# Performance work log

Hardware: AMD Instinct MI355X
Metric: run time of the kernel (lower is better)

## Reference

```python
import jax, jax.numpy as jnp
import numpy as np

D = 256    # lstm_encoder_size
B = 1024   # batch (number of agents/trajectories)
T = 512    # prediction horizon (recurrence steps)
EPS = 1e-5


def setup_inputs() -> dict:
    key = jax.random.key(0)
    k = jax.random.split(key, 10)
    s = 1.0 / np.sqrt(D)
    return {
        "KS_ALL": jax.random.normal(k[0], (1, B, D), jnp.float32),
        "next_vf": jax.random.normal(k[1], (B, T), jnp.float32),
        # Koopman operators (torch Linear stores [out, in]; no bias)
        "A_w": jax.random.normal(k[2], (D, D), jnp.float32) * (0.4 * s),  # contractive
        "B_w": jax.random.normal(k[3], (D, 1), jnp.float32) * s,
        # decoder params (liner_dec=False)
        "W0": jax.random.normal(k[4], (2 * D, D), jnp.float32) * s,
        "b0": jnp.zeros((2 * D,), jnp.float32),
        "W1": jax.random.normal(k[5], (D, 2 * D), jnp.float32) / np.sqrt(2.0 * D),
        "b1": jnp.zeros((D,), jnp.float32),
        "ln_g": jnp.ones((D,), jnp.float32),
        "ln_b": jnp.zeros((D,), jnp.float32),
        "W2": jax.random.normal(k[6], (D, D), jnp.float32) * s,
        "b2": jnp.zeros((D,), jnp.float32),
        "W3": jax.random.normal(k[7], (3, D), jnp.float32) * s,
        "b3": jnp.zeros((3,), jnp.float32),
    }


def _layer_norm(x, g, b):
    mu = jnp.mean(x, axis=-1, keepdims=True)
    var = jnp.var(x, axis=-1, keepdims=True)
    return (x - mu) * jax.lax.rsqrt(var + EPS) * g + b


def reference(KS_ALL, next_vf, A_w, B_w, W0, b0, W1, b1, ln_g, ln_b, W2, b2, W3, b3):
    # train_flag=True -> use only the first time slice of KS_ALL
    ks0 = KS_ALL[0]                 # [B, D]
    u = next_vf.T                   # [T, B] time-major, matches permute(1,0,2)
    b_vec = B_w[:, 0]               # [D]  (Linear(1, D) on scalar input)

    def step(ks, u_t):
        ks_new = ks @ A_w.T + u_t[:, None] * b_vec[None, :]  # [B, D]
        return ks_new, ks_new

    _, ks_seq = jax.lax.scan(step, ks0, u)                   # [T, B, D]
    KS_pre = jnp.concatenate([ks0[None], ks_seq], axis=0)    # [T+1, B, D]

    # nonlinear decoder (eval mode: dropout is identity; use_elu=True)
    s1 = jnp.tanh(KS_pre @ W0.T + b0)          # [T+1, B, 2D]
    s2 = jnp.tanh(s1 @ W1.T + b1)              # [T+1, B, D]
    s2 = _layer_norm(KS_pre + s2, ln_g, ln_b)  # AddAndNorm
    s3 = jax.nn.elu(s2 @ W2.T + b2)
    OS = s3 @ W3.T + b3                        # [T+1, B, 3]
    return KS_pre, OS
```

## Files before the change

### kernel.cpp

```cpp
#include <hip/hip_runtime.h>

typedef unsigned short u16;
typedef __attribute__((ext_vector_type(8))) short bf16x8;
typedef __attribute__((ext_vector_type(4))) short bf16x4;
typedef __attribute__((ext_vector_type(4))) float f32x4;

#define MFMA16(a, b, c) __builtin_amdgcn_mfma_f32_16x16x32_bf16((a), (b), (c), 0, 0, 0)

#define OFF_UPAD 0
#define OFF_KS0  589824
#define OFF_W0   851968
#define OFF_W1   983040
#define OFF_W2   1114112
#define OFF_CRT  1179648
#define OFF_P    1196032
#define OS_OFF   134479872

__device__ __forceinline__ u16 f2bf(float f) {
  union { float f; unsigned int i; } v; v.f = f;
  return (u16)((v.i + 0x7fffu + ((v.i >> 16) & 1u)) >> 16);
}
__device__ __forceinline__ float bf2f(u16 u) {
  union { unsigned int i; float f; } v; v.i = ((unsigned int)u) << 16;
  return v.f;
}
__device__ __forceinline__ float fast_tanh(float x) {
  float e = __expf(2.0f * x);
  return 1.0f - __fdividef(2.0f, e + 1.0f);
}

__global__ void k_prep(const float* __restrict__ KS_ALL, const float* __restrict__ next_vf,
                       const float* __restrict__ A_w, const float* __restrict__ W0,
                       const float* __restrict__ W1, const float* __restrict__ W2,
                       u16* __restrict__ ws) {
  int idx = blockIdx.x * 256 + threadIdx.x;
  if (idx < 589824) {
    int r = idx / 576, c = idx % 576;
    ws[OFF_UPAD + idx] = (c < 64) ? (u16)0 : f2bf(next_vf[r * 512 + c - 64]);
    return;
  }
  idx -= 589824;
  if (idx < 262144) { ws[OFF_KS0 + idx] = f2bf(KS_ALL[idx]); return; }
  idx -= 262144;
  if (idx < 131072) { ws[OFF_W0 + idx] = f2bf(W0[idx]); return; }
  idx -= 131072;
  if (idx < 131072) { ws[OFF_W1 + idx] = f2bf(W1[idx]); return; }
  idx -= 131072;
  if (idx < 65536)  { ws[OFF_W2 + idx] = f2bf(W2[idx]); return; }
  idx -= 65536;
  if (idx < 65536) {
    int r = idx >> 8, c = idx & 255;
    ws[OFF_P + idx] = (r == c) ? (u16)0x3F80 : (u16)0;
    ws[OFF_P + 65536 + idx] = f2bf(A_w[idx]);
  }
}

__global__ __launch_bounds__(512) void k_pow(u16* __restrict__ ws, int s) {
  const u16* P = ws + OFF_P;
  int j = blockIdx.y + 1;
  int mh = blockIdx.x;
  int lane = threadIdx.x & 63, w = threadIdx.x >> 6;
  int wm = w >> 2, wn = w & 3;
  int lg = lane >> 4, ll = lane & 15;
  const u16* Am = P + s * 65536;
  const u16* Bm = P + j * 65536;
  f32x4 acc[4][4];
  f32x4 z = {0.f, 0.f, 0.f, 0.f};
#pragma unroll
  for (int mi = 0; mi < 4; ++mi)
#pragma unroll
    for (int ni = 0; ni < 4; ++ni) acc[mi][ni] = z;
#pragma unroll
  for (int ks = 0; ks < 8; ++ks) {
    bf16x8 a[4], b[4];
    int kk = ks * 32 + lg * 8;
#pragma unroll
    for (int mi = 0; mi < 4; ++mi) {
      int row = mh * 128 + wm * 64 + mi * 16 + ll;
      a[mi] = *(const bf16x8*)(Am + row * 256 + kk);
    }
#pragma unroll
    for (int ni = 0; ni < 4; ++ni) {
      int col = wn * 64 + ni * 16 + ll;
#pragma unroll
      for (int e = 0; e < 8; ++e) b[ni][e] = (short)Bm[(kk + e) * 256 + col];
    }
#pragma unroll
    for (int mi = 0; mi < 4; ++mi)
#pragma unroll
      for (int ni = 0; ni < 4; ++ni) acc[mi][ni] = MFMA16(a[mi], b[ni], acc[mi][ni]);
  }
  u16* Pd = ws + OFF_P + (s + j) * 65536;
#pragma unroll
  for (int mi = 0; mi < 4; ++mi)
#pragma unroll
    for (int ni = 0; ni < 4; ++ni)
#pragma unroll
      for (int r = 0; r < 4; ++r) {
        int row = mh * 128 + wm * 64 + mi * 16 + lg * 4 + r;
        int col = wn * 64 + ni * 16 + ll;
        Pd[row * 256 + col] = f2bf(acc[mi][ni][r]);
      }
}

__global__ void k_crevt(const float* __restrict__ B_w, u16* __restrict__ ws) {
  int s = blockIdx.x;
  int n = threadIdx.x;
  const u16* Pr = ws + OFF_P + (63 - s) * 65536 + n * 256;
  float acc = 0.f;
  for (int k = 0; k < 256; ++k) acc += bf2f(Pr[k]) * B_w[k];
  ws[OFF_CRT + n * 64 + s] = f2bf(acc);
}

__global__ __launch_bounds__(512) void k_fused(
    const u16* __restrict__ ws,
    const float* __restrict__ b0, const float* __restrict__ b1,
    const float* __restrict__ lng, const float* __restrict__ lnb,
    const float* __restrict__ b2, const float* __restrict__ W3,
    const float* __restrict__ b3, float* __restrict__ out) {
  __shared__ __align__(16) u16 Xb[16896];
  __shared__ __align__(16) unsigned char Hraw[33792];
  __shared__ float par[2308];
  u16* Hb = (u16*)Hraw;
  float* Hf = (float*)Hraw;

  float* pb0 = par;
  float* pb1 = par + 512;
  float* pg  = par + 768;
  float* pbt = par + 1024;
  float* pb2 = par + 1280;
  float* pW3 = par + 1536;
  float* pb3 = par + 2304;

  const int t  = blockIdx.y;
  const int R0 = blockIdx.x * 64;
  const int tid = threadIdx.x;
  const int lane = tid & 63, w = tid >> 6;
  const int lg = lane >> 4, ll = lane & 15;

  pb0[tid] = b0[tid];
  if (tid < 256) { pb1[tid] = b1[tid]; pg[tid] = lng[tid]; pbt[tid] = lnb[tid]; pb2[tid] = b2[tid]; }
  if (tid < 512) pW3[tid] = W3[tid];
  if (tid < 256) pW3[512 + tid] = W3[512 + tid];
  if (tid < 4) pb3[tid] = (tid < 3) ? b3[tid] : 0.f;

  f32x4 z = {0.f, 0.f, 0.f, 0.f};

  f32x4 acc[4][2];
#pragma unroll
  for (int mi = 0; mi < 4; ++mi)
#pragma unroll
    for (int ni = 0; ni < 2; ++ni) acc[mi][ni] = z;
  {
    const u16* CrevT = ws + OFF_CRT;
#pragma unroll
    for (int ksu = 0; ksu < 2; ++ksu) {
      bf16x8 au[4];
#pragma unroll
      for (int mi = 0; mi < 4; ++mi) {
        const u16* up = ws + OFF_UPAD + (R0 + mi * 16 + ll) * 576 + t + ksu * 32 + lg * 8;
#pragma unroll
        for (int e = 0; e < 8; ++e) au[mi][e] = (short)up[e];
      }
#pragma unroll
      for (int ni = 0; ni < 2; ++ni) {
        int n = w * 32 + ni * 16 + ll;
        bf16x8 bfr = *(const bf16x8*)(CrevT + n * 64 + ksu * 32 + lg * 8);
#pragma unroll
        for (int mi = 0; mi < 4; ++mi) acc[mi][ni] = MFMA16(au[mi], bfr, acc[mi][ni]);
      }
    }
    if (t < 64) {
      const u16* Pt = ws + OFF_P + t * 65536;
      const u16* ks0b = ws + OFF_KS0;
#pragma unroll
      for (int ks = 0; ks < 8; ++ks) {
        bf16x8 a[4], b[2];
#pragma unroll
        for (int mi = 0; mi < 4; ++mi)
          a[mi] = *(const bf16x8*)(ks0b + (R0 + mi * 16 + ll) * 256 + ks * 32 + lg * 8);
#pragma unroll
        for (int ni = 0; ni < 2; ++ni)
          b[ni] = *(const bf16x8*)(Pt + (w * 32 + ni * 16 + ll) * 256 + ks * 32 + lg * 8);
#pragma unroll
        for (int mi = 0; mi < 4; ++mi)
#pragma unroll
          for (int ni = 0; ni < 2; ++ni) acc[mi][ni] = MFMA16(a[mi], b[ni], acc[mi][ni]);
      }
    }
  }

#pragma unroll 1
  for (int p = 0; p < 2; ++p) {
#pragma unroll
    for (int mi2 = 0; mi2 < 2; ++mi2) {
      int mi = p * 2 + mi2;
#pragma unroll
      for (int ni = 0; ni < 2; ++ni)
#pragma unroll
        for (int r = 0; r < 4; ++r)
          Hf[(mi2 * 16 + lg * 4 + r) * 260 + w * 32 + ni * 16 + ll] = acc[mi][ni][r];
    }
    __syncthreads();
    float* ob = out + (size_t)t * 262144 + (size_t)(R0 + p * 32) * 256;
#pragma unroll
    for (int it = 0; it < 4; ++it) {
      int idx = it * 512 + tid;
      int row = idx >> 6, c4 = idx & 63;
      f32x4 v = *(const f32x4*)(Hf + row * 260 + c4 * 4);
      *(f32x4*)(ob + row * 256 + c4 * 4) = v;
      int rl = p * 32 + row;
      bf16x4 h;
#pragma unroll
      for (int e = 0; e < 4; ++e) h[e] = (short)f2bf(v[e]);
      int byt = (((rl << 9) + ((c4 >> 1) << 4)) ^ ((rl & 7) << 4)) + ((c4 & 1) << 3);
      *(bf16x4*)(Xb + (byt >> 1)) = h;
    }
    __syncthreads();
  }

  const u16* W0b = ws + OFF_W0;
  const u16* W1b = ws + OFF_W1;
  f32x4 accL2[4][2];
#pragma unroll
  for (int mi = 0; mi < 4; ++mi)
#pragma unroll
    for (int ni = 0; ni < 2; ++ni) accL2[mi][ni] = z;

  const int colL1 = w * 16 + ll;
#pragma unroll 1
  for (int q = 0; q < 4; ++q) {
    f32x4 accQ[4];
#pragma unroll
    for (int mi = 0; mi < 4; ++mi) accQ[mi] = z;
#pragma unroll
    for (int ks = 0; ks < 8; ++ks) {
      bf16x8 b = *(const bf16x8*)(W0b + (q * 128 + colL1) * 256 + ks * 32 + lg * 8);
#pragma unroll
      for (int mi = 0; mi < 4; ++mi) {
        int rl = mi * 16 + ll;
        int byt = ((rl << 9) + ks * 64 + (lg << 4)) ^ ((rl & 7) << 4);
        bf16x8 a = *(const bf16x8*)(Xb + (byt >> 1));
        accQ[mi] = MFMA16(a, b, accQ[mi]);
      }
    }
#pragma unroll
    for (int mi = 0; mi < 4; ++mi)
#pragma unroll
      for (int r = 0; r < 4; ++r) {
        int rl2 = mi * 16 + lg * 4 + r;
        float v = fast_tanh(accQ[mi][r] + pb0[q * 128 + colL1]);
        int byt = ((rl2 << 8) + (colL1 << 1)) ^ ((rl2 & 7) << 4);
        Hb[byt >> 1] = f2bf(v);
      }
    __syncthreads();
#pragma unroll
    for (int ks2 = 0; ks2 < 4; ++ks2) {
      bf16x8 bf0 = *(const bf16x8*)(W1b + (w * 32 + ll) * 512 + q * 128 + ks2 * 32 + lg * 8);
      bf16x8 bf1 = *(const bf16x8*)(W1b + (w * 32 + 16 + ll) * 512 + q * 128 + ks2 * 32 + lg * 8);
#pragma unroll
      for (int mi = 0; mi < 4; ++mi) {
        int rl = mi * 16 + ll;
        int byt = ((rl << 8) + ks2 * 64 + (lg << 4)) ^ ((rl & 7) << 4);
        bf16x8 a = *(const bf16x8*)(Hb + (byt >> 1));
        accL2[mi][0] = MFMA16(a, bf0, accL2[mi][0]);
        accL2[mi][1] = MFMA16(a, bf1, accL2[mi][1]);
      }
    }
    __syncthreads();
  }

#pragma unroll
  for (int mi = 0; mi < 4; ++mi)
#pragma unroll
    for (int ni = 0; ni < 2; ++ni)
#pragma unroll
      for (int r = 0; r < 4; ++r) {
        int rl = mi * 16 + lg * 4 + r;
        int col = w * 32 + ni * 16 + ll;
        float v = fast_tanh(accL2[mi][ni][r] + pb1[col]);
        int bx = ((rl << 9) + (col << 1)) ^ ((rl & 7) << 4);
        v += bf2f(Xb[bx >> 1]);
        Hb[rl * 264 + col] = f2bf(v);
      }
  __syncthreads();

  {
    int row = tid >> 3, jq = tid & 7;
    u16* hr = Hb + row * 264 + jq * 32;
    bf16x8 chv[4];
#pragma unroll
    for (int q = 0; q < 4; ++q) chv[q] = *(const bf16x8*)(hr + q * 8);
    float s = 0.f, ss = 0.f;
#pragma unroll
    for (int q = 0; q < 4; ++q)
#pragma unroll
      for (int e = 0; e < 8; ++e) { float v = bf2f((u16)chv[q][e]); s += v; ss += v * v; }
    s += __shfl_xor(s, 1);  s += __shfl_xor(s, 2);  s += __shfl_xor(s, 4);
    ss += __shfl_xor(ss, 1); ss += __shfl_xor(ss, 2); ss += __shfl_xor(ss, 4);
    float mu = s * 0.00390625f;
    float var = ss * 0.00390625f - mu * mu;
    float rstd = rsqrtf(var + 1e-5f);
#pragma unroll
    for (int q = 0; q < 4; ++q) {
      bf16x8 o;
#pragma unroll
      for (int e = 0; e < 8; ++e) {
        int col = jq * 32 + q * 8 + e;
        float v = (bf2f((u16)chv[q][e]) - mu) * rstd * pg[col] + pbt[col];
        o[e] = (short)f2bf(v);
      }
      *(bf16x8*)(hr + q * 8) = o;
    }
  }
  __syncthreads();

  {
    const u16* W2b = ws + OFF_W2;
    f32x4 a3[4][2];
#pragma unroll
    for (int mi = 0; mi < 4; ++mi)
#pragma unroll
      for (int ni = 0; ni < 2; ++ni) a3[mi][ni] = z;
#pragma unroll
    for (int ks = 0; ks < 8; ++ks) {
      bf16x8 bf0 = *(const bf16x8*)(W2b + (w * 32 + ll) * 256 + ks * 32 + lg * 8);
      bf16x8 bf1 = *(const bf16x8*)(W2b + (w * 32 + 16 + ll) * 256 + ks * 32 + lg * 8);
#pragma unroll
      for (int mi = 0; mi < 4; ++mi) {
        int rl = mi * 16 + ll;
        bf16x8 a = *(const bf16x8*)(Hb + rl * 264 + ks * 32 + lg * 8);
        a3[mi][0] = MFMA16(a, bf0, a3[mi][0]);
        a3[mi][1] = MFMA16(a, bf1, a3[mi][1]);
      }
    }
#pragma unroll
    for (int mi = 0; mi < 4; ++mi)
#pragma unroll
      for (int ni = 0; ni < 2; ++ni)
#pragma unroll
        for (int r = 0; r < 4; ++r) {
          int rl = mi * 16 + lg * 4 + r;
          int col = w * 32 + ni * 16 + ll;
          float v = a3[mi][ni][r] + pb2[col];
          v = v > 0.f ? v : (__expf(v) - 1.f);
          Xb[rl * 264 + col] = f2bf(v);
        }
  }
  __syncthreads();

  {
    int row = tid >> 3, jq = tid & 7;
    const u16* xr = Xb + row * 264 + jq * 32;
    float d0 = 0.f, d1 = 0.f, d2 = 0.f;
#pragma unroll
    for (int q = 0; q < 4; ++q) {
      bf16x8 c = *(const bf16x8*)(xr + q * 8);
#pragma unroll
      for (int e = 0; e < 8; ++e) {
        float v = bf2f((u16)c[e]);
        int col = jq * 32 + q * 8 + e;
        d0 += v * pW3[col]; d1 += v * pW3[256 + col]; d2 += v * pW3[512 + col];
      }
    }
    d0 += __shfl_xor(d0, 1); d0 += __shfl_xor(d0, 2); d0 += __shfl_xor(d0, 4);
    d1 += __shfl_xor(d1, 1); d1 += __shfl_xor(d1, 2); d1 += __shfl_xor(d1, 4);
    d2 += __shfl_xor(d2, 1); d2 += __shfl_xor(d2, 2); d2 += __shfl_xor(d2, 4);
    if (jq == 0) {
      int grow = R0 + row;
      int ob = OS_OFF + t * 3072 + grow * 3;
      out[ob]     = d0 + pb3[0];
      out[ob + 1] = d1 + pb3[1];
      out[ob + 2] = d2 + pb3[2];
    }
  }
}

extern "C" void kernel_launch(void* const* d_in, const int* in_sizes, int n_in,
                              void* d_out, int out_size, void* d_ws, size_t ws_size,
                              hipStream_t stream) {
  const float* KS_ALL  = (const float*)d_in[0];
  const float* next_vf = (const float*)d_in[1];
  const float* A_w     = (const float*)d_in[2];
  const float* B_w     = (const float*)d_in[3];
  const float* W0      = (const float*)d_in[4];
  const float* b0      = (const float*)d_in[5];
  const float* W1      = (const float*)d_in[6];
  const float* b1      = (const float*)d_in[7];
  const float* lng     = (const float*)d_in[8];
  const float* lnb     = (const float*)d_in[9];
  const float* W2      = (const float*)d_in[10];
  const float* b2      = (const float*)d_in[11];
  const float* W3      = (const float*)d_in[12];
  const float* b3      = (const float*)d_in[13];
  u16* ws = (u16*)d_ws;
  float* out = (float*)d_out;

  k_prep<<<4864, 256, 0, stream>>>(KS_ALL, next_vf, A_w, W0, W1, W2, ws);
  for (int s = 1; s <= 32; s <<= 1)
    k_pow<<<dim3(2, s), 512, 0, stream>>>(ws, s);
  k_crevt<<<64, 256, 0, stream>>>(B_w, ws);
  k_fused<<<dim3(16, 513), 512, 0, stream>>>(ws, b0, b1, lng, lnb, b2, W3, b3, out);
}
```

Measured before the change: 1.604 ms.

## Split fused decoder kernel into KS, layer1, layer2, layer3 kernels over time chunks

Replaces the single fused kernel with a KS-sequence kernel and three per-layer decoder kernels, run over four time chunks. Intermediates (tanh layer-1 output, layer-normed activations) are staged in bf16 workspace buffers. The aim is lower register and LDS pressure per kernel, for higher occupancy and simpler GEMM tiles. The cost is extra global memory traffic for the intermediates, a re-read of the fp32 KS output, and more kernel launches. The path only runs when the workspace is large enough.

After: 1.613 ms. No clear change (+0.6%).

```diff
diff --git a/kernel.cpp b/kernel.cpp
--- a/kernel.cpp
+++ b/kernel.cpp
@@ -14,6 +14,9 @@
 #define OFF_W2   1114112
 #define OFF_CRT  1179648
 #define OFF_P    1196032
+#define OFF_H1   5455872
+#define OFF_S2   73089024
+#define WS_END_U16 106905600ULL
 #define OS_OFF   134479872
 
 __device__ __forceinline__ u16 f2bf(float f) {
@@ -112,6 +115,387 @@
   ws[OFF_CRT + n * 64 + s] = f2bf(acc);
 }
 
+
+__global__ __launch_bounds__(512) void k_ks(const u16* __restrict__ ws, float* __restrict__ out) {
+  __shared__ __align__(16) float Hf[32 * 260];
+  const int t  = blockIdx.y;
+  const int R0 = blockIdx.x * 64;
+  const int tid = threadIdx.x;
+  const int lane = tid & 63, w = tid >> 6;
+  const int lg = lane >> 4, ll = lane & 15;
+  f32x4 z = {0.f, 0.f, 0.f, 0.f};
+
+  f32x4 acc[4][2];
+#pragma unroll
+  for (int mi = 0; mi < 4; ++mi)
+#pragma unroll
+    for (int ni = 0; ni < 2; ++ni) acc[mi][ni] = z;
+  {
+    const u16* CrevT = ws + OFF_CRT;
+#pragma unroll
+    for (int ksu = 0; ksu < 2; ++ksu) {
+      bf16x8 au[4];
+#pragma unroll
+      for (int mi = 0; mi < 4; ++mi) {
+        const u16* up = ws + OFF_UPAD + (R0 + mi * 16 + ll) * 576 + t + ksu * 32 + lg * 8;
+#pragma unroll
+        for (int e = 0; e < 8; ++e) au[mi][e] = (short)up[e];
+      }
+#pragma unroll
+      for (int ni = 0; ni < 2; ++ni) {
+        int n = w * 32 + ni * 16 + ll;
+        bf16x8 bfr = *(const bf16x8*)(CrevT + n * 64 + ksu * 32 + lg * 8);
+#pragma unroll
+        for (int mi = 0; mi < 4; ++mi) acc[mi][ni] = MFMA16(au[mi], bfr, acc[mi][ni]);
+      }
+    }
+    if (t < 64) {
+      const u16* Pt = ws + OFF_P + t * 65536;
+      const u16* ks0b = ws + OFF_KS0;
+#pragma unroll
+      for (int ks = 0; ks < 8; ++ks) {
+        bf16x8 a[4], b[2];
+#pragma unroll
+        for (int mi = 0; mi < 4; ++mi)
+          a[mi] = *(const bf16x8*)(ks0b + (R0 + mi * 16 + ll) * 256 + ks * 32 + lg * 8);
+#pragma unroll
+        for (int ni = 0; ni < 2; ++ni)
+          b[ni] = *(const bf16x8*)(Pt + (w * 32 + ni * 16 + ll) * 256 + ks * 32 + lg * 8);
+#pragma unroll
+        for (int mi = 0; mi < 4; ++mi)
+#pragma unroll
+          for (int ni = 0; ni < 2; ++ni) acc[mi][ni] = MFMA16(a[mi], b[ni], acc[mi][ni]);
+      }
+    }
+  }
+#pragma unroll 1
+  for (int p = 0; p < 2; ++p) {
+#pragma unroll
+    for (int mi2 = 0; mi2 < 2; ++mi2) {
+      int mi = p * 2 + mi2;
+#pragma unroll
+      for (int ni = 0; ni < 2; ++ni)
+#pragma unroll
+        for (int r = 0; r < 4; ++r)
+          Hf[(mi2 * 16 + lg * 4 + r) * 260 + w * 32 + ni * 16 + ll] = acc[mi][ni][r];
+    }
+    __syncthreads();
+    float* ob = out + (size_t)t * 262144 + (size_t)(R0 + p * 32) * 256;
+#pragma unroll
+    for (int it = 0; it < 4; ++it) {
+      int idx = it * 512 + tid;
+      int row = idx >> 6, c4 = idx & 63;
+      f32x4 v = *(const f32x4*)(Hf + row * 260 + c4 * 4);
+      *(f32x4*)(ob + row * 256 + c4 * 4) = v;
+    }
+    __syncthreads();
+  }
+}
+
+__global__ __launch_bounds__(512) void k_l1(const u16* __restrict__ ws,
+                                            const float* __restrict__ outf,
+                                            const float* __restrict__ b0,
+                                            u16* __restrict__ h1, int t0) {
+  __shared__ __align__(16) u16 Xb[16896];
+  __shared__ __align__(16) u16 Hb[16896];
+  __shared__ float pb0s[512];
+  const int by = blockIdx.y;
+  const int t  = t0 + by;
+  const int R0 = blockIdx.x * 64;
+  const int tid = threadIdx.x;
+  const int lane = tid & 63, w = tid >> 6;
+  const int lg = lane >> 4, ll = lane & 15;
+  f32x4 z = {0.f, 0.f, 0.f, 0.f};
+
+  pb0s[tid] = b0[tid];
+  {
+    const float* xs = outf + (size_t)t * 262144 + (size_t)R0 * 256;
+#pragma unroll
+    for (int it = 0; it < 8; ++it) {
+      int idx = it * 512 + tid;
+      int row = idx >> 6, c4 = idx & 63;
+      f32x4 v = *(const f32x4*)(xs + row * 256 + c4 * 4);
+      bf16x4 h;
+#pragma unroll
+      for (int e = 0; e < 4; ++e) h[e] = (short)f2bf(v[e]);
+      int byt = (((row << 9) + ((c4 >> 1) << 4)) ^ ((row & 7) << 4)) + ((c4 & 1) << 3);
+      *(bf16x4*)(Xb + (byt >> 1)) = h;
+    }
+  }
+  __syncthreads();
+
+  const u16* W0b = ws + OFF_W0;
+#pragma unroll 1
+  for (int nh = 0; nh < 2; ++nh) {
+    f32x4 acc[4][2];
+#pragma unroll
+    for (int mi = 0; mi < 4; ++mi)
+#pragma unroll
+      for (int ni = 0; ni < 2; ++ni) acc[mi][ni] = z;
+#pragma unroll
+    for (int ks = 0; ks < 8; ++ks) {
+      bf16x8 b[2];
+#pragma unroll
+      for (int ni = 0; ni < 2; ++ni) {
+        int n = nh * 256 + w * 32 + ni * 16 + ll;
+        b[ni] = *(const bf16x8*)(W0b + n * 256 + ks * 32 + lg * 8);
+      }
+#pragma unroll
+      for (int mi = 0; mi < 4; ++mi) {
+        int rl = mi * 16 + ll;
+        int byt = ((rl << 9) + ks * 64 + (lg << 4)) ^ ((rl & 7) << 4);
+        bf16x8 a = *(const bf16x8*)(Xb + (byt >> 1));
+#pragma unroll
+        for (int ni = 0; ni < 2; ++ni) acc[mi][ni] = MFMA16(a, b[ni], acc[mi][ni]);
+      }
+    }
+#pragma unroll
+    for (int mi = 0; mi < 4; ++mi)
+#pragma unroll
+      for (int ni = 0; ni < 2; ++ni)
+#pragma unroll
+        for (int r = 0; r < 4; ++r) {
+          int rl = mi * 16 + lg * 4 + r;
+          int col = w * 32 + ni * 16 + ll;
+          Hb[rl * 264 + col] = f2bf(fast_tanh(acc[mi][ni][r] + pb0s[nh * 256 + col]));
+        }
+    __syncthreads();
+    u16* hd = h1 + ((size_t)(by * 1024 + R0)) * 512 + nh * 256;
+#pragma unroll
+    for (int it = 0; it < 4; ++it) {
+      int idx = it * 512 + tid;
+      int row = idx >> 5, cq = idx & 31;
+      bf16x8 v = *(const bf16x8*)(Hb + row * 264 + cq * 8);
+      *(bf16x8*)(hd + row * 512 + cq * 8) = v;
+    }
+    __syncthreads();
+  }
+}
+
+__global__ __launch_bounds__(512) void k_l2(const u16* __restrict__ ws,
+                                            const float* __restrict__ outf,
+                                            const float* __restrict__ b1,
+                                            const float* __restrict__ lng,
+                                            const float* __restrict__ lnb,
+                                            const u16* __restrict__ h1,
+                                            u16* __restrict__ s2, int t0) {
+  __shared__ __align__(16) u16 Hs[16896];
+  __shared__ __align__(16) u16 Rb[16896];
+  __shared__ float par[768];
+  float* pb1 = par;
+  float* pg  = par + 256;
+  float* pbt = par + 512;
+  const int by = blockIdx.y;
+  const int t  = t0 + by;
+  const int R0 = blockIdx.x * 64;
+  const int tid = threadIdx.x;
+  const int lane = tid & 63, w = tid >> 6;
+  const int lg = lane >> 4, ll = lane & 15;
+  f32x4 z = {0.f, 0.f, 0.f, 0.f};
+
+  if (tid < 256) { pb1[tid] = b1[tid]; pg[tid] = lng[tid]; pbt[tid] = lnb[tid]; }
+
+  f32x4 accL2[4][2];
+#pragma unroll
+  for (int mi = 0; mi < 4; ++mi)
+#pragma unroll
+    for (int ni = 0; ni < 2; ++ni) accL2[mi][ni] = z;
+
+  const u16* W1b = ws + OFF_W1;
+  const u16* h1b = h1 + ((size_t)(by * 1024 + R0)) * 512;
+#pragma unroll 1
+  for (int kh = 0; kh < 2; ++kh) {
+#pragma unroll
+    for (int it = 0; it < 4; ++it) {
+      int idx = it * 512 + tid;
+      int row = idx >> 5, cq = idx & 31;
+      bf16x8 v = *(const bf16x8*)(h1b + row * 512 + kh * 256 + cq * 8);
+      int byt = ((row << 9) + (cq << 4)) ^ ((row & 7) << 4);
+      *(bf16x8*)(Hs + (byt >> 1)) = v;
+    }
+    __syncthreads();
+#pragma unroll
+    for (int ks = 0; ks < 8; ++ks) {
+      bf16x8 b[2];
+#pragma unroll
+      for (int ni = 0; ni < 2; ++ni) {
+        int n = w * 32 + ni * 16 + ll;
+        b[ni] = *(const bf16x8*)(W1b + n * 512 + kh * 256 + ks * 32 + lg * 8);
+      }
+#pragma unroll
+      for (int mi = 0; mi < 4; ++mi) {
+        int rl = mi * 16 + ll;
+        int byt = ((rl << 9) + ks * 64 + (lg << 4)) ^ ((rl & 7) << 4);
+        bf16x8 a = *(const bf16x8*)(Hs + (byt >> 1));
+#pragma unroll
+        for (int ni = 0; ni < 2; ++ni) accL2[mi][ni] = MFMA16(a, b[ni], accL2[mi][ni]);
+      }
+    }
+    __syncthreads();
+  }
+
+  {
+    const float* xs = outf + (size_t)t * 262144 + (size_t)R0 * 256;
+#pragma unroll
+    for (int mi = 0; mi < 4; ++mi)
+#pragma unroll
+      for (int ni = 0; ni < 2; ++ni)
+#pragma unroll
+        for (int r = 0; r < 4; ++r) {
+          int rl = mi * 16 + lg * 4 + r;
+          int col = w * 32 + ni * 16 + ll;
+          float v = xs[rl * 256 + col] + fast_tanh(accL2[mi][ni][r] + pb1[col]);
+          Rb[rl * 264 + col] = f2bf(v);
+        }
+  }
+  __syncthreads();
+
+  {
+    int row = tid >> 3, jq = tid & 7;
+    u16* hr = Rb + row * 264 + jq * 32;
+    bf16x8 chv[4];
+#pragma unroll
+    for (int q = 0; q < 4; ++q) chv[q] = *(const bf16x8*)(hr + q * 8);
+    float s = 0.f, ss = 0.f;
+#pragma unroll
+    for (int q = 0; q < 4; ++q)
+#pragma unroll
+      for (int e = 0; e < 8; ++e) { float v = bf2f((u16)chv[q][e]); s += v; ss += v * v; }
+    s += __shfl_xor(s, 1);  s += __shfl_xor(s, 2);  s += __shfl_xor(s, 4);
+    ss += __shfl_xor(ss, 1); ss += __shfl_xor(ss, 2); ss += __shfl_xor(ss, 4);
+    float mu = s * 0.00390625f;
+    float var = ss * 0.00390625f - mu * mu;
+    float rstd = rsqrtf(var + 1e-5f);
+#pragma unroll
+    for (int q = 0; q < 4; ++q) {
+      bf16x8 o;
+#pragma unroll
+      for (int e = 0; e < 8; ++e) {
+        int col = jq * 32 + q * 8 + e;
+        float v = (bf2f((u16)chv[q][e]) - mu) * rstd * pg[col] + pbt[col];
+        o[e] = (short)f2bf(v);
+      }
+      *(bf16x8*)(hr + q * 8) = o;
+    }
+  }
+  __syncthreads();
+
+  {
+    u16* sd = s2 + ((size_t)(by * 1024 + R0)) * 256;
+#pragma unroll
+    for (int it = 0; it < 4; ++it) {
+      int idx = it * 512 + tid;
+      int row = idx >> 5, cq = idx & 31;
+      bf16x8 v = *(const bf16x8*)(Rb + row * 264 + cq * 8);
+      *(bf16x8*)(sd + row * 256 + cq * 8) = v;
+    }
+  }
+}
+
+__global__ __launch_bounds__(512) void k_l3(const u16* __restrict__ ws,
+                                            const float* __restrict__ b2,
+                                            const float* __restrict__ W3,
+                                            const float* __restrict__ b3,
+                                            const u16* __restrict__ s2,
+                                            float* __restrict__ out, int t0) {
+  __shared__ __align__(16) u16 Sb[16896];
+  __shared__ __align__(16) u16 Eb[16896];
+  __shared__ float par[1028];
+  float* pb2 = par;
+  float* pW3 = par + 256;
+  float* pb3 = par + 1024;
+  const int by = blockIdx.y;
+  const int t  = t0 + by;
+  const int R0 = blockIdx.x * 64;
+  const int tid = threadIdx.x;
+  const int lane = tid & 63, w = tid >> 6;
+  const int lg = lane >> 4, ll = lane & 15;
+  f32x4 z = {0.f, 0.f, 0.f, 0.f};
+
+  if (tid < 256) pb2[tid] = b2[tid];
+  if (tid < 512) pW3[tid] = W3[tid];
+  if (tid < 256) pW3[512 + tid] = W3[512 + tid];
+  if (tid < 4) pb3[tid] = (tid < 3) ? b3[tid] : 0.f;
+
+  {
+    const u16* sb = s2 + ((size_t)(by * 1024 + R0)) * 256;
+#pragma unroll
+    for (int it = 0; it < 4; ++it) {
+      int idx = it * 512 + tid;
+      int row = idx >> 5, cq = idx & 31;
+      bf16x8 v = *(const bf16x8*)(sb + row * 256 + cq * 8);
+      int byt = ((row << 9) + (cq << 4)) ^ ((row & 7) << 4);
+      *(bf16x8*)(Sb + (byt >> 1)) = v;
+    }
+  }
+  __syncthreads();
+
+  f32x4 acc[4][2];
+#pragma unroll
+  for (int mi = 0; mi < 4; ++mi)
+#pragma unroll
+    for (int ni = 0; ni < 2; ++ni) acc[mi][ni] = z;
+  {
+    const u16* W2b = ws + OFF_W2;
+#pragma unroll
+    for (int ks = 0; ks < 8; ++ks) {
+      bf16x8 b[2];
+#pragma unroll
+      for (int ni = 0; ni < 2; ++ni) {
+        int n = w * 32 + ni * 16 + ll;
+        b[ni] = *(const bf16x8*)(W2b + n * 256 + ks * 32 + lg * 8);
+      }
+#pragma unroll
+      for (int mi = 0; mi < 4; ++mi) {
+        int rl = mi * 16 + ll;
+        int byt = ((rl << 9) + ks * 64 + (lg << 4)) ^ ((rl & 7) << 4);
+        bf16x8 a = *(const bf16x8*)(Sb + (byt >> 1));
+#pragma unroll
+        for (int ni = 0; ni < 2; ++ni) acc[mi][ni] = MFMA16(a, b[ni], acc[mi][ni]);
+      }
+    }
+  }
+#pragma unroll
+  for (int mi = 0; mi < 4; ++mi)
+#pragma unroll
+    for (int ni = 0; ni < 2; ++ni)
+#pragma unroll
+      for (int r = 0; r < 4; ++r) {
+        int rl = mi * 16 + lg * 4 + r;
+        int col = w * 32 + ni * 16 + ll;
+        float v = acc[mi][ni][r] + pb2[col];
+        v = v > 0.f ? v : (__expf(v) - 1.f);
+        Eb[rl * 264 + col] = f2bf(v);
+      }
+  __syncthreads();
+
+  {
+    int row = tid >> 3, jq = tid & 7;
+    const u16* xr = Eb + row * 264 + jq * 32;
+    float d0 = 0.f, d1 = 0.f, d2 = 0.f;
+#pragma unroll
+    for (int q = 0; q < 4; ++q) {
+      bf16x8 c = *(const bf16x8*)(xr + q * 8);
+#pragma unroll
+      for (int e = 0; e < 8; ++e) {
+        float v = bf2f((u16)c[e]);
+        int col = jq * 32 + q * 8 + e;
+        d0 += v * pW3[col]; d1 += v * pW3[256 + col]; d2 += v * pW3[512 + col];
+      }
+    }
+    d0 += __shfl_xor(d0, 1); d0 += __shfl_xor(d0, 2); d0 += __shfl_xor(d0, 4);
+    d1 += __shfl_xor(d1, 1); d1 += __shfl_xor(d1, 2); d1 += __shfl_xor(d1, 4);
+    d2 += __shfl_xor(d2, 1); d2 += __shfl_xor(d2, 2); d2 += __shfl_xor(d2, 4);
+    if (jq == 0) {
+      int grow = R0 + row;
+      int ob = OS_OFF + t * 3072 + grow * 3;
+      out[ob]     = d0 + pb3[0];
+      out[ob + 1] = d1 + pb3[1];
+      out[ob + 2] = d2 + pb3[2];
+    }
+  }
+}
+
 __global__ __launch_bounds__(512) void k_fused(
     const u16* __restrict__ ws,
     const float* __restrict__ b0, const float* __restrict__ b1,
@@ -123,7 +507,6 @@
   __shared__ float par[2308];
   u16* Hb = (u16*)Hraw;
   float* Hf = (float*)Hraw;
-
   float* pb0 = par;
   float* pb1 = par + 512;
   float* pg  = par + 768;
@@ -131,21 +514,17 @@
   float* pb2 = par + 1280;
   float* pW3 = par + 1536;
   float* pb3 = par + 2304;
-
   const int t  = blockIdx.y;
   const int R0 = blockIdx.x * 64;
   const int tid = threadIdx.x;
   const int lane = tid & 63, w = tid >> 6;
   const int lg = lane >> 4, ll = lane & 15;
-
   pb0[tid] = b0[tid];
   if (tid < 256) { pb1[tid] = b1[tid]; pg[tid] = lng[tid]; pbt[tid] = lnb[tid]; pb2[tid] = b2[tid]; }
   if (tid < 512) pW3[tid] = W3[tid];
   if (tid < 256) pW3[512 + tid] = W3[512 + tid];
   if (tid < 4) pb3[tid] = (tid < 3) ? b3[tid] : 0.f;
-
   f32x4 z = {0.f, 0.f, 0.f, 0.f};
-
   f32x4 acc[4][2];
 #pragma unroll
   for (int mi = 0; mi < 4; ++mi)
@@ -189,7 +568,6 @@
       }
     }
   }
-
 #pragma unroll 1
   for (int p = 0; p < 2; ++p) {
 #pragma unroll
@@ -218,7 +596,6 @@
     }
     __syncthreads();
   }
-
   const u16* W0b = ws + OFF_W0;
   const u16* W1b = ws + OFF_W1;
   f32x4 accL2[4][2];
@@ -226,7 +603,6 @@
   for (int mi = 0; mi < 4; ++mi)
 #pragma unroll
     for (int ni = 0; ni < 2; ++ni) accL2[mi][ni] = z;
-
   const int colL1 = w * 16 + ll;
 #pragma unroll 1
   for (int q = 0; q < 4; ++q) {
@@ -269,7 +645,6 @@
     }
     __syncthreads();
   }
-
 #pragma unroll
   for (int mi = 0; mi < 4; ++mi)
 #pragma unroll
@@ -284,7 +659,6 @@
         Hb[rl * 264 + col] = f2bf(v);
       }
   __syncthreads();
-
   {
     int row = tid >> 3, jq = tid & 7;
     u16* hr = Hb + row * 264 + jq * 32;
@@ -314,7 +688,6 @@
     }
   }
   __syncthreads();
-
   {
     const u16* W2b = ws + OFF_W2;
     f32x4 a3[4][2];
@@ -348,7 +721,6 @@
         }
   }
   __syncthreads();
-
   {
     int row = tid >> 3, jq = tid & 7;
     const u16* xr = Xb + row * 264 + jq * 32;
@@ -400,5 +772,19 @@
   for (int s = 1; s <= 32; s <<= 1)
     k_pow<<<dim3(2, s), 512, 0, stream>>>(ws, s);
   k_crevt<<<64, 256, 0, stream>>>(B_w, ws);
-  k_fused<<<dim3(16, 513), 512, 0, stream>>>(ws, b0, b1, lng, lnb, b2, W3, b3, out);
-}
+
+  if (ws_size >= WS_END_U16 * 2ULL) {
+    k_ks<<<dim3(16, 513), 512, 0, stream>>>(ws, out);
+    u16* h1 = ws + OFF_H1;
+    u16* s2 = ws + OFF_S2;
+    const int t0s[4] = {0, 129, 257, 385};
+    const int nts[4] = {129, 128, 128, 128};
+    for (int c = 0; c < 4; ++c) {
+      k_l1<<<dim3(16, nts[c]), 512, 0, stream>>>(ws, out, b0, h1, t0s[c]);
+      k_l2<<<dim3(16, nts[c]), 512, 0, stream>>>(ws, out, b1, lng, lnb, h1, s2, t0s[c]);
+      k_l3<<<dim3(16, nts[c]), 512, 0, stream>>>(ws, b2, W3, b3, s2, out, t0s[c]);
+    }
+  } else {
+    k_fused<<<dim3(16, 513), 512, 0, stream>>>(ws, b0, b1, lng, lnb, b2, W3, b3, out);
+  }
+}
```

## Split fused kernel into KS-generation and MLP kernels with aligned u copies

Applied to the files above, without the earlier changes.

Splits the single fused kernel into one kernel that computes and stores the KS trajectory and a second that reloads it from global memory to run the decoder MLP. Precomputes eight shifted copies of the padded input so the u-window loads become aligned 16-byte vector loads. LDS use drops by reusing Xb for the residual and layer-norm stages, and the OS output is staged in shared memory for coalesced nontemporal stores. In exchange it adds a global round-trip of the roughly 537 MB KS tensor and a larger prep kernel.

Measured after the change: 1.503 ms. 1.07x faster.

```diff
diff --git a/kernel.cpp b/kernel.cpp
--- a/kernel.cpp
+++ b/kernel.cpp
@@ -7,13 +7,14 @@
 
 #define MFMA16(a, b, c) __builtin_amdgcn_mfma_f32_16x16x32_bf16((a), (b), (c), 0, 0, 0)
 
-#define OFF_UPAD 0
-#define OFF_KS0  589824
-#define OFF_W0   851968
-#define OFF_W1   983040
-#define OFF_W2   1114112
-#define OFF_CRT  1179648
-#define OFF_P    1196032
+#define OFF_U8   0
+#define U8_CPY   598016
+#define OFF_KS0  4784128
+#define OFF_W0   5046272
+#define OFF_W1   5177344
+#define OFF_W2   5308416
+#define OFF_CRT  5373952
+#define OFF_P    5390336
 #define OS_OFF   134479872
 
 __device__ __forceinline__ u16 f2bf(float f) {
@@ -34,12 +35,16 @@
                        const float* __restrict__ W1, const float* __restrict__ W2,
                        u16* __restrict__ ws) {
   int idx = blockIdx.x * 256 + threadIdx.x;
-  if (idx < 589824) {
-    int r = idx / 576, c = idx % 576;
-    ws[OFF_UPAD + idx] = (c < 64) ? (u16)0 : f2bf(next_vf[r * 512 + c - 64]);
+  if (idx < 4784128) {
+    int p = idx / U8_CPY;
+    int rem = idx - p * U8_CPY;
+    int b = rem / 584;
+    int c = rem - b * 584;
+    int col = c + p;
+    ws[OFF_U8 + idx] = (col >= 64 && col < 576) ? f2bf(next_vf[b * 512 + col - 64]) : (u16)0;
     return;
   }
-  idx -= 589824;
+  idx -= 4784128;
   if (idx < 262144) { ws[OFF_KS0 + idx] = f2bf(KS_ALL[idx]); return; }
   idx -= 262144;
   if (idx < 131072) { ws[OFF_W0 + idx] = f2bf(W0[idx]); return; }
@@ -112,18 +117,94 @@
   ws[OFF_CRT + n * 64 + s] = f2bf(acc);
 }
 
-__global__ __launch_bounds__(512) void k_fused(
-    const u16* __restrict__ ws,
-    const float* __restrict__ b0, const float* __restrict__ b1,
-    const float* __restrict__ lng, const float* __restrict__ lnb,
-    const float* __restrict__ b2, const float* __restrict__ W3,
-    const float* __restrict__ b3, float* __restrict__ out) {
+__global__ __launch_bounds__(512) void k_ks(const u16* __restrict__ ws, float* __restrict__ out) {
+  __shared__ __align__(16) float Hf[32 * 260];
+  const int t  = blockIdx.y;
+  const int R0 = blockIdx.x * 64;
+  const int tid = threadIdx.x;
+  const int lane = tid & 63, w = tid >> 6;
+  const int lg = lane >> 4, ll = lane & 15;
+  f32x4 z = {0.f, 0.f, 0.f, 0.f};
+
+  f32x4 acc[4][2];
+#pragma unroll
+  for (int mi = 0; mi < 4; ++mi)
+#pragma unroll
+    for (int ni = 0; ni < 2; ++ni) acc[mi][ni] = z;
+  {
+    const u16* CrevT = ws + OFF_CRT;
+    const u16* u8b = ws + OFF_U8 + (size_t)(t & 7) * U8_CPY + (t & ~7);
+#pragma unroll
+    for (int ksu = 0; ksu < 2; ++ksu) {
+      bf16x8 au[4];
+#pragma unroll
+      for (int mi = 0; mi < 4; ++mi)
+        au[mi] = *(const bf16x8*)(u8b + (R0 + mi * 16 + ll) * 584 + ksu * 32 + lg * 8);
+#pragma unroll
+      for (int ni = 0; ni < 2; ++ni) {
+        int n = w * 32 + ni * 16 + ll;
+        bf16x8 bfr = *(const bf16x8*)(CrevT + n * 64 + ksu * 32 + lg * 8);
+#pragma unroll
+        for (int mi = 0; mi < 4; ++mi) acc[mi][ni] = MFMA16(au[mi], bfr, acc[mi][ni]);
+      }
+    }
+    if (t < 64) {
+      const u16* Pt = ws + OFF_P + t * 65536;
+      const u16* ks0b = ws + OFF_KS0;
+#pragma unroll
+      for (int ks = 0; ks < 8; ++ks) {
+        bf16x8 a[4], b[2];
+#pragma unroll
+        for (int mi = 0; mi < 4; ++mi)
+          a[mi] = *(const bf16x8*)(ks0b + (R0 + mi * 16 + ll) * 256 + ks * 32 + lg * 8);
+#pragma unroll
+        for (int ni = 0; ni < 2; ++ni)
+          b[ni] = *(const bf16x8*)(Pt + (w * 32 + ni * 16 + ll) * 256 + ks * 32 + lg * 8);
+#pragma unroll
+        for (int mi = 0; mi < 4; ++mi)
+#pragma unroll
+          for (int ni = 0; ni < 2; ++ni) acc[mi][ni] = MFMA16(a[mi], b[ni], acc[mi][ni]);
+      }
+    }
+  }
+#pragma unroll 1
+  for (int p = 0; p < 2; ++p) {
+#pragma unroll
+    for (int mi2 = 0; mi2 < 2; ++mi2) {
+      int mi = p * 2 + mi2;
+#pragma unroll
+      for (int ni = 0; ni < 2; ++ni)
+#pragma unroll
+        for (int r = 0; r < 4; ++r)
+          Hf[(mi2 * 16 + lg * 4 + r) * 260 + w * 32 + ni * 16 + ll] = acc[mi][ni][r];
+    }
+    __syncthreads();
+    float* ob = out + (size_t)t * 262144 + (size_t)(R0 + p * 32) * 256;
+#pragma unroll
+    for (int it = 0; it < 4; ++it) {
+      int idx = it * 512 + tid;
+      int row = idx >> 6, c4 = idx & 63;
+      f32x4 v = *(const f32x4*)(Hf + row * 260 + c4 * 4);
+      __builtin_nontemporal_store(v, (f32x4*)(ob + row * 256 + c4 * 4));
+    }
+    __syncthreads();
+  }
+}
+
+__global__ __launch_bounds__(512) void k_mlp(const u16* __restrict__ ws,
+                                             const float* __restrict__ outf,
+                                             const float* __restrict__ b0,
+                                             const float* __restrict__ b1,
+                                             const float* __restrict__ lng,
+                                             const float* __restrict__ lnb,
+                                             const float* __restrict__ b2,
+                                             const float* __restrict__ W3,
+                                             const float* __restrict__ b3,
+                                             float* __restrict__ out) {
   __shared__ __align__(16) u16 Xb[16896];
-  __shared__ __align__(16) unsigned char Hraw[33792];
+  __shared__ __align__(16) u16 Hs[8448];
   __shared__ float par[2308];
-  u16* Hb = (u16*)Hraw;
-  float* Hf = (float*)Hraw;
-
+  __shared__ float osb[208];
   float* pb0 = par;
   float* pb1 = par + 512;
   float* pg  = par + 768;
@@ -131,12 +212,12 @@
   float* pb2 = par + 1280;
   float* pW3 = par + 1536;
   float* pb3 = par + 2304;
-
   const int t  = blockIdx.y;
   const int R0 = blockIdx.x * 64;
   const int tid = threadIdx.x;
   const int lane = tid & 63, w = tid >> 6;
   const int lg = lane >> 4, ll = lane & 15;
+  f32x4 z = {0.f, 0.f, 0.f, 0.f};
 
   pb0[tid] = b0[tid];
   if (tid < 256) { pb1[tid] = b1[tid]; pg[tid] = lng[tid]; pbt[tid] = lnb[tid]; pb2[tid] = b2[tid]; }
@@ -144,80 +225,21 @@
   if (tid < 256) pW3[512 + tid] = W3[512 + tid];
   if (tid < 4) pb3[tid] = (tid < 3) ? b3[tid] : 0.f;
 
-  f32x4 z = {0.f, 0.f, 0.f, 0.f};
-
-  f32x4 acc[4][2];
-#pragma unroll
-  for (int mi = 0; mi < 4; ++mi)
-#pragma unroll
-    for (int ni = 0; ni < 2; ++ni) acc[mi][ni] = z;
   {
-    const u16* CrevT = ws + OFF_CRT;
-#pragma unroll
-    for (int ksu = 0; ksu < 2; ++ksu) {
-      bf16x8 au[4];
-#pragma unroll
-      for (int mi = 0; mi < 4; ++mi) {
-        const u16* up = ws + OFF_UPAD + (R0 + mi * 16 + ll) * 576 + t + ksu * 32 + lg * 8;
-#pragma unroll
-        for (int e = 0; e < 8; ++e) au[mi][e] = (short)up[e];
-      }
-#pragma unroll
-      for (int ni = 0; ni < 2; ++ni) {
-        int n = w * 32 + ni * 16 + ll;
-        bf16x8 bfr = *(const bf16x8*)(CrevT + n * 64 + ksu * 32 + lg * 8);
-#pragma unroll
-        for (int mi = 0; mi < 4; ++mi) acc[mi][ni] = MFMA16(au[mi], bfr, acc[mi][ni]);
-      }
-    }
-    if (t < 64) {
-      const u16* Pt = ws + OFF_P + t * 65536;
-      const u16* ks0b = ws + OFF_KS0;
-#pragma unroll
-      for (int ks = 0; ks < 8; ++ks) {
-        bf16x8 a[4], b[2];
-#pragma unroll
-        for (int mi = 0; mi < 4; ++mi)
-          a[mi] = *(const bf16x8*)(ks0b + (R0 + mi * 16 + ll) * 256 + ks * 32 + lg * 8);
-#pragma unroll
-        for (int ni = 0; ni < 2; ++ni)
-          b[ni] = *(const bf16x8*)(Pt + (w * 32 + ni * 16 + ll) * 256 + ks * 32 + lg * 8);
-#pragma unroll
-        for (int mi = 0; mi < 4; ++mi)
-#pragma unroll
-          for (int ni = 0; ni < 2; ++ni) acc[mi][ni] = MFMA16(a[mi], b[ni], acc[mi][ni]);
-      }
-    }
-  }
-
-#pragma unroll 1
-  for (int p = 0; p < 2; ++p) {
-#pragma unroll
-    for (int mi2 = 0; mi2 < 2; ++mi2) {
-      int mi = p * 2 + mi2;
-#pragma unroll
-      for (int ni = 0; ni < 2; ++ni)
-#pragma unroll
-        for (int r = 0; r < 4; ++r)
-          Hf[(mi2 * 16 + lg * 4 + r) * 260 + w * 32 + ni * 16 + ll] = acc[mi][ni][r];
-    }
-    __syncthreads();
-    float* ob = out + (size_t)t * 262144 + (size_t)(R0 + p * 32) * 256;
-#pragma unroll
-    for (int it = 0; it < 4; ++it) {
+    const float* xs = outf + (size_t)t * 262144 + (size_t)R0 * 256;
+#pragma unroll
+    for (int it = 0; it < 8; ++it) {
       int idx = it * 512 + tid;
       int row = idx >> 6, c4 = idx & 63;
-      f32x4 v = *(const f32x4*)(Hf + row * 260 + c4 * 4);
-      *(f32x4*)(ob + row * 256 + c4 * 4) = v;
-      int rl = p * 32 + row;
+      f32x4 v = __builtin_nontemporal_load((const f32x4*)(xs + row * 256 + c4 * 4));
       bf16x4 h;
 #pragma unroll
       for (int e = 0; e < 4; ++e) h[e] = (short)f2bf(v[e]);
-      int byt = (((rl << 9) + ((c4 >> 1) << 4)) ^ ((rl & 7) << 4)) + ((c4 & 1) << 3);
+      int byt = (((row << 9) + ((c4 >> 1) << 4)) ^ ((row & 7) << 4)) + ((c4 & 1) << 3);
       *(bf16x4*)(Xb + (byt >> 1)) = h;
     }
-    __syncthreads();
-  }
+  }
+  __syncthreads();
 
   const u16* W0b = ws + OFF_W0;
   const u16* W1b = ws + OFF_W1;
@@ -226,7 +248,6 @@
   for (int mi = 0; mi < 4; ++mi)
 #pragma unroll
     for (int ni = 0; ni < 2; ++ni) accL2[mi][ni] = z;
-
   const int colL1 = w * 16 + ll;
 #pragma unroll 1
   for (int q = 0; q < 4; ++q) {
@@ -251,7 +272,7 @@
         int rl2 = mi * 16 + lg * 4 + r;
         float v = fast_tanh(accQ[mi][r] + pb0[q * 128 + colL1]);
         int byt = ((rl2 << 8) + (colL1 << 1)) ^ ((rl2 & 7) << 4);
-        Hb[byt >> 1] = f2bf(v);
+        Hs[byt >> 1] = f2bf(v);
       }
     __syncthreads();
 #pragma unroll
@@ -262,7 +283,7 @@
       for (int mi = 0; mi < 4; ++mi) {
         int rl = mi * 16 + ll;
         int byt = ((rl << 8) + ks2 * 64 + (lg << 4)) ^ ((rl & 7) << 4);
-        bf16x8 a = *(const bf16x8*)(Hb + (byt >> 1));
+        bf16x8 a = *(const bf16x8*)(Hs + (byt >> 1));
         accL2[mi][0] = MFMA16(a, bf0, accL2[mi][0]);
         accL2[mi][1] = MFMA16(a, bf1, accL2[mi][1]);
       }
@@ -278,19 +299,21 @@
       for (int r = 0; r < 4; ++r) {
         int rl = mi * 16 + lg * 4 + r;
         int col = w * 32 + ni * 16 + ll;
-        float v = fast_tanh(accL2[mi][ni][r] + pb1[col]);
         int bx = ((rl << 9) + (col << 1)) ^ ((rl & 7) << 4);
-        v += bf2f(Xb[bx >> 1]);
-        Hb[rl * 264 + col] = f2bf(v);
+        float v = bf2f(Xb[bx >> 1]) + fast_tanh(accL2[mi][ni][r] + pb1[col]);
+        Xb[bx >> 1] = f2bf(v);
       }
   __syncthreads();
 
   {
     int row = tid >> 3, jq = tid & 7;
-    u16* hr = Hb + row * 264 + jq * 32;
     bf16x8 chv[4];
-#pragma unroll
-    for (int q = 0; q < 4; ++q) chv[q] = *(const bf16x8*)(hr + q * 8);
+    int byts[4];
+#pragma unroll
+    for (int q = 0; q < 4; ++q) {
+      byts[q] = ((row << 9) + ((jq * 32 + q * 8) << 1)) ^ ((row & 7) << 4);
+      chv[q] = *(const bf16x8*)(Xb + (byts[q] >> 1));
+    }
     float s = 0.f, ss = 0.f;
 #pragma unroll
     for (int q = 0; q < 4; ++q)
@@ -310,18 +333,18 @@
         float v = (bf2f((u16)chv[q][e]) - mu) * rstd * pg[col] + pbt[col];
         o[e] = (short)f2bf(v);
       }
-      *(bf16x8*)(hr + q * 8) = o;
-    }
-  }
-  __syncthreads();
-
+      *(bf16x8*)(Xb + (byts[q] >> 1)) = o;
+    }
+  }
+  __syncthreads();
+
+  f32x4 a3[4][2];
+#pragma unroll
+  for (int mi = 0; mi < 4; ++mi)
+#pragma unroll
+    for (int ni = 0; ni < 2; ++ni) a3[mi][ni] = z;
   {
     const u16* W2b = ws + OFF_W2;
-    f32x4 a3[4][2];
-#pragma unroll
-    for (int mi = 0; mi < 4; ++mi)
-#pragma unroll
-      for (int ni = 0; ni < 2; ++ni) a3[mi][ni] = z;
 #pragma unroll
     for (int ks = 0; ks < 8; ++ks) {
       bf16x8 bf0 = *(const bf16x8*)(W2b + (w * 32 + ll) * 256 + ks * 32 + lg * 8);
@@ -329,24 +352,26 @@
 #pragma unroll
       for (int mi = 0; mi < 4; ++mi) {
         int rl = mi * 16 + ll;
-        bf16x8 a = *(const bf16x8*)(Hb + rl * 264 + ks * 32 + lg * 8);
+        int byt = ((rl << 9) + ks * 64 + (lg << 4)) ^ ((rl & 7) << 4);
+        bf16x8 a = *(const bf16x8*)(Xb + (byt >> 1));
         a3[mi][0] = MFMA16(a, bf0, a3[mi][0]);
         a3[mi][1] = MFMA16(a, bf1, a3[mi][1]);
       }
     }
-#pragma unroll
-    for (int mi = 0; mi < 4; ++mi)
-#pragma unroll
-      for (int ni = 0; ni < 2; ++ni)
-#pragma unroll
-        for (int r = 0; r < 4; ++r) {
-          int rl = mi * 16 + lg * 4 + r;
-          int col = w * 32 + ni * 16 + ll;
-          float v = a3[mi][ni][r] + pb2[col];
-          v = v > 0.f ? v : (__expf(v) - 1.f);
-          Xb[rl * 264 + col] = f2bf(v);
-        }
-  }
+  }
+  __syncthreads();
+#pragma unroll
+  for (int mi = 0; mi < 4; ++mi)
+#pragma unroll
+    for (int ni = 0; ni < 2; ++ni)
+#pragma unroll
+      for (int r = 0; r < 4; ++r) {
+        int rl = mi * 16 + lg * 4 + r;
+        int col = w * 32 + ni * 16 + ll;
+        float v = a3[mi][ni][r] + pb2[col];
+        v = v > 0.f ? v : (__expf(v) - 1.f);
+        Xb[rl * 264 + col] = f2bf(v);
+      }
   __syncthreads();
 
   {
@@ -367,12 +392,15 @@
     d1 += __shfl_xor(d1, 1); d1 += __shfl_xor(d1, 2); d1 += __shfl_xor(d1, 4);
     d2 += __shfl_xor(d2, 1); d2 += __shfl_xor(d2, 2); d2 += __shfl_xor(d2, 4);
     if (jq == 0) {
-      int grow = R0 + row;
-      int ob = OS_OFF + t * 3072 + grow * 3;
-      out[ob]     = d0 + pb3[0];
-      out[ob + 1] = d1 + pb3[1];
-      out[ob + 2] = d2 + pb3[2];
-    }
+      osb[row * 3]     = d0 + pb3[0];
+      osb[row * 3 + 1] = d1 + pb3[1];
+      osb[row * 3 + 2] = d2 + pb3[2];
+    }
+  }
+  __syncthreads();
+  if (tid < 48) {
+    f32x4 v = *(const f32x4*)(osb + tid * 4);
+    __builtin_nontemporal_store(v, (f32x4*)(out + OS_OFF + (size_t)t * 3072 + (size_t)R0 * 3 + tid * 4));
   }
 }
 
@@ -396,9 +424,11 @@
   u16* ws = (u16*)d_ws;
   float* out = (float*)d_out;
 
-  k_prep<<<4864, 256, 0, stream>>>(KS_ALL, next_vf, A_w, W0, W1, W2, ws);
+  k_prep<<<21248, 256, 0, stream>>>(KS_ALL, next_vf, A_w, W0, W1, W2, ws);
   for (int s = 1; s <= 32; s <<= 1)
     k_pow<<<dim3(2, s), 512, 0, stream>>>(ws, s);
   k_crevt<<<64, 256, 0, stream>>>(B_w, ws);
-  k_fused<<<dim3(16, 513), 512, 0, stream>>>(ws, b0, b1, lng, lnb, b2, W3, b3, out);
-}
+
+  k_ks<<<dim3(16, 513), 512, 0, stream>>>(ws, out);
+  k_mlp<<<dim3(16, 513), 512, 0, stream>>>(ws, out, b0, b1, lng, lnb, b2, W3, b3, out);
+}
```
